# Optimization experiments

Measured on AMD Instinct MI355X. Metric: run time of the kernel, lower is better.

## Reference

```python
import jax, jax.numpy as jnp
import numpy as np

G, N, F, H, B, L = 4, 1024, 256, 256, 32, 4


def setup_inputs() -> dict:
    key = jax.random.key(0)
    ks = jax.random.split(key, 8)
    batch_xs = jax.random.normal(ks[0], (G, N, F), dtype=jnp.float32)
    # dense (preprocessed/normalized) adjacency; scale ~1/N keeps activations stable
    batch_as = jax.random.uniform(ks[1], (G, N, N), dtype=jnp.float32) / N
    w_in = jax.random.normal(ks[2], (F, H), dtype=jnp.float32) * 0.05
    b_in = jnp.zeros((H,), dtype=jnp.float32)
    gcn_w = jax.random.normal(ks[3], (L, H, H), dtype=jnp.float32) * 0.05
    gcn_b = jnp.zeros((L, H), dtype=jnp.float32)
    graph_idx = jax.random.randint(ks[4], (B,), 0, G)
    cp_mask = jax.random.randint(ks[5], (B, N), 0, 2).astype(bool)
    return {"batch_xs": batch_xs, "batch_as": batch_as, "w_in": w_in, "b_in": b_in,
            "gcn_w": gcn_w, "gcn_b": gcn_b, "graph_idx": graph_idx, "cp_mask": cp_mask}


def reference(batch_xs, batch_as, w_in, b_in, gcn_w, gcn_b, graph_idx, cp_mask):
    # gather_nd: select per-example graph features and adjacency
    X = batch_xs[graph_idx]          # [B, N, F]
    A = batch_as[graph_idx]          # [B, N, N]
    # GNN input dense layer (relu); dropout is identity at inference
    x = jax.nn.relu(X @ w_in + b_in)  # [B, N, H]
    res = x                           # residual from post-input activations
    # GCNConv stack: act(A @ x @ W + b); relu for all but final tanh layer
    for i in range(L - 1):
        x = jax.nn.relu(jnp.einsum('bnm,bmh->bnh', A, x) @ gcn_w[i] + gcn_b[i])
    x = jnp.tanh(jnp.einsum('bnm,bmh->bnh', A, x) @ gcn_w[L - 1] + gcn_b[L - 1])
    x = x + res
    # ragged boolean_mask + reduce_mean over nodes == masked mean
    m = cp_mask.astype(x.dtype)       # [B, N]
    denom = jnp.maximum(jnp.sum(m, axis=1, keepdims=True), 1.0)
    return jnp.sum(x * m[..., None], axis=1) / denom  # [B, H]
```

## Files before the change

kernel.cpp:

```cpp
#include <hip/hip_runtime.h>
#include <math.h>

#define G 4
#define NN 1024
#define FF 256
#define HH 256
#define BB 32
#define LL 4

typedef __attribute__((ext_vector_type(8))) short short8;
typedef __attribute__((ext_vector_type(8))) unsigned short ushort8;
typedef __attribute__((ext_vector_type(4))) unsigned short ushort4v;
typedef __attribute__((ext_vector_type(4))) float floatx4;

__device__ inline unsigned short f2bf(float f) {
  union { float f; unsigned u; } x; x.f = f;
  unsigned r = x.u + 0x7fffu + ((x.u >> 16) & 1u);
  return (unsigned short)(r >> 16);
}

template <int ACT, int AMODE, int OMODE, int SPLITK>
__global__ __launch_bounds__(256) void gemm(
    const void* __restrict__ Aptr, long aStride, long a2Off,
    const float* __restrict__ biasA,
    const unsigned short* __restrict__ Bt, long bStride,
    const float* __restrict__ biasC,
    unsigned short* __restrict__ outT,
    unsigned short* __restrict__ outBf,
    float* __restrict__ outF,
    int Kb, int ldA, int ldB) {
  __shared__ __align__(16) unsigned short As[64 * 72];
  __shared__ __align__(16) unsigned short Bs[64 * 72];

  const int z = blockIdx.z;
  const int g = (SPLITK == 2) ? (z & 3) : z;
  const int koff = (SPLITK == 2) ? (z >> 2) * Kb : 0;
  const int m0 = blockIdx.y * 64;
  const int n0 = blockIdx.x * 64;
  const int t = threadIdx.x;
  const int lane = t & 63, w = t >> 6;
  const int wm = w & 1, wn = w >> 1;
  const int l16 = lane & 15, quad = lane >> 4;

  const unsigned short* Bg = Bt + (long)g * bStride;

  ushort8 pa[2], pb[2];
  float4 pf[2][4];

  auto load_tile = [&](int tt) {
    const int kb = koff + tt * 64;
#pragma unroll
    for (int i = 0; i < 2; ++i) {
      const int q = t + i * 256;
      const int row = q >> 3, c8 = q & 7;
      if (AMODE == 0) {
        const unsigned short* Ab =
            (const unsigned short*)Aptr + (long)g * aStride;
        pa[i] = *(const ushort8*)&Ab[(long)(m0 + row) * ldA + kb + c8 * 8];
      } else {
        const float* Af = (const float*)Aptr + (long)g * aStride +
                          (long)(m0 + row) * ldA + kb + c8 * 8;
        pf[i][0] = *(const float4*)Af;
        pf[i][1] = *(const float4*)(Af + 4);
        if (AMODE == 2) {
          pf[i][2] = *(const float4*)(Af + a2Off);
          pf[i][3] = *(const float4*)(Af + a2Off + 4);
        }
      }
      pb[i] = *(const ushort8*)&Bg[(long)(n0 + row) * ldB + kb + c8 * 8];
    }
  };

  auto store_tile = [&](int tt) {
    const int kb = koff + tt * 64;
#pragma unroll
    for (int i = 0; i < 2; ++i) {
      const int q = t + i * 256;
      const int row = q >> 3, c8 = q & 7;
      ushort8 v;
      if (AMODE == 0) {
        v = pa[i];
      } else {
        float a[8] = {pf[i][0].x, pf[i][0].y, pf[i][0].z, pf[i][0].w,
                      pf[i][1].x, pf[i][1].y, pf[i][1].z, pf[i][1].w};
        if (AMODE == 2) {
          float a2[8] = {pf[i][2].x, pf[i][2].y, pf[i][2].z, pf[i][2].w,
                         pf[i][3].x, pf[i][3].y, pf[i][3].z, pf[i][3].w};
          float4 bb0 = *(const float4*)&biasA[kb + c8 * 8];
          float4 bb1 = *(const float4*)&biasA[kb + c8 * 8 + 4];
          float bb[8] = {bb0.x, bb0.y, bb0.z, bb0.w,
                         bb1.x, bb1.y, bb1.z, bb1.w};
#pragma unroll
          for (int j = 0; j < 8; ++j) a[j] = fmaxf(a[j] + a2[j] + bb[j], 0.f);
        }
#pragma unroll
        for (int j = 0; j < 8; ++j) v[j] = f2bf(a[j]);
      }
      *(ushort8*)&As[row * 72 + c8 * 8] = v;
      *(ushort8*)&Bs[row * 72 + c8 * 8] = pb[i];
    }
  };

  floatx4 acc[2][2];
#pragma unroll
  for (int i = 0; i < 2; ++i)
#pragma unroll
    for (int j = 0; j < 2; ++j) acc[i][j] = (floatx4){0.f, 0.f, 0.f, 0.f};

  const int nt = Kb / 64;
  load_tile(0);
  for (int tt = 0; tt < nt; ++tt) {
    __syncthreads();
    store_tile(tt);
    __syncthreads();
    if (tt + 1 < nt) load_tile(tt + 1);
#pragma unroll
    for (int kk = 0; kk < 64; kk += 32) {
      const int ko = kk + quad * 8;
      short8 a0 = *(const short8*)&As[(wm * 32 + l16) * 72 + ko];
      short8 a1 = *(const short8*)&As[(wm * 32 + 16 + l16) * 72 + ko];
      short8 b0 = *(const short8*)&Bs[(wn * 32 + l16) * 72 + ko];
      short8 b1 = *(const short8*)&Bs[(wn * 32 + 16 + l16) * 72 + ko];
      acc[0][0] = __builtin_amdgcn_mfma_f32_16x16x32_bf16(a0, b0, acc[0][0], 0, 0, 0);
      acc[0][1] = __builtin_amdgcn_mfma_f32_16x16x32_bf16(a0, b1, acc[0][1], 0, 0, 0);
      acc[1][0] = __builtin_amdgcn_mfma_f32_16x16x32_bf16(a1, b0, acc[1][0], 0, 0, 0);
      acc[1][1] = __builtin_amdgcn_mfma_f32_16x16x32_bf16(a1, b1, acc[1][1], 0, 0, 0);
    }
  }

  const int zc = (SPLITK == 2) ? z : g;
#pragma unroll
  for (int i = 0; i < 2; ++i) {
#pragma unroll
    for (int j = 0; j < 2; ++j) {
      const int n = n0 + wn * 32 + j * 16 + l16;
      const int mB = m0 + wm * 32 + i * 16 + quad * 4;
      const float bv = biasC ? biasC[n] : 0.f;
      ushort4v pv;
#pragma unroll
      for (int r = 0; r < 4; ++r) {
        float v = acc[i][j][r] + bv;
        if (ACT == 1) v = fmaxf(v, 0.f);
        if (OMODE & 4) outF[(long)zc * NN * HH + (long)(mB + r) * HH + n] = v;
        if (OMODE & 3) pv[r] = f2bf(v);
        if (OMODE & 2)
          outBf[(long)g * NN * HH + (long)(mB + r) * HH + n] = pv[r];
      }
      if (OMODE & 1)
        *(ushort4v*)&outT[(long)g * HH * NN + (long)n * NN + mB] = pv;
    }
  }
}

__global__ __launch_bounds__(256) void pre_kernel(
    const float* __restrict__ batch_as, unsigned short* __restrict__ Abf,
    const float* __restrict__ w_in, unsigned short* __restrict__ winT,
    const float* __restrict__ gcn_w, unsigned short* __restrict__ gwT,
    const void* __restrict__ mask_raw, float* __restrict__ fmask,
    float* __restrict__ denom, float* __restrict__ out) {
  const int b = blockIdx.x;
  const int t = threadIdx.x;
  if (b < 1024) {
    const long idx = ((long)b * 256 + t) * 16;
#pragma unroll
    for (int h = 0; h < 2; ++h) {
      float4 f0 = *(const float4*)&batch_as[idx + h * 8];
      float4 f1 = *(const float4*)&batch_as[idx + h * 8 + 4];
      ushort8 v;
      v[0] = f2bf(f0.x); v[1] = f2bf(f0.y); v[2] = f2bf(f0.z);
      v[3] = f2bf(f0.w); v[4] = f2bf(f1.x); v[5] = f2bf(f1.y);
      v[6] = f2bf(f1.z); v[7] = f2bf(f1.w);
      *(ushort8*)&Abf[idx + h * 8] = v;
    }
  } else if (b < 2304) {
    const int b2 = b - 1024;
    const int mat = b2 >> 8;
    const int rb = b2 & 255;
    const float* src = (mat == 0) ? w_in : gcn_w + (long)(mat - 1) * HH * HH;
    unsigned short* dst = (mat == 0) ? winT : gwT + (long)(mat - 1) * HH * HH;
    dst[rb * 256 + t] = f2bf(src[t * 256 + rb]);
  } else {
    const int bb = b - 2304;
    const unsigned char* bytes = (const unsigned char*)mask_raw;
    out[bb * HH + t] = 0.f;
    __shared__ int fmt;
    if (t == 0) {
      int any = 0;
      for (int i = 0; i < 256; ++i)
        if ((i & 3) && bytes[i]) any = 1;
      fmt = any ? 0 : 1;
    }
    __syncthreads();
    float cnt = 0.f;
    for (int n = t; n < NN; n += 256) {
      float v;
      if (fmt)
        v = ((const int*)mask_raw)[bb * NN + n] ? 1.f : 0.f;
      else
        v = bytes[bb * NN + n] ? 1.f : 0.f;
      fmask[bb * NN + n] = v;
      cnt += v;
    }
    __shared__ float red[256];
    red[t] = cnt;
    __syncthreads();
    for (int s = 128; s > 0; s >>= 1) {
      if (t < s) red[t] += red[t + s];
      __syncthreads();
    }
    if (t == 0) denom[bb] = fmaxf(red[0], 1.f);
  }
}

__global__ __launch_bounds__(256) void mean_kernel(
    const float* __restrict__ T0, const float* __restrict__ T1,
    const float* __restrict__ bias3, const float* __restrict__ h0f,
    const float* __restrict__ fmask, const float* __restrict__ denom,
    const int* __restrict__ gidx, float* __restrict__ out) {
  const int b = blockIdx.x >> 4;
  const int ch = blockIdx.x & 15;
  const int h = threadIdx.x;
  const int g = gidx[b];
  const long base = (long)g * NN * HH;
  const float bv = bias3[h];
  const int n0 = ch * 64;
  float s = 0.f;
  for (int n = n0; n < n0 + 64; ++n) {
    float m = fmask[b * NN + n];
    if (m != 0.f) {
      const long idx = base + (long)n * HH + h;
      s += tanhf(T0[idx] + T1[idx] + bv) + h0f[idx];
    }
  }
  atomicAdd(&out[b * HH + h], s / denom[b]);
}

extern "C" void kernel_launch(void* const* d_in, const int* in_sizes, int n_in,
                              void* d_out, int out_size, void* d_ws,
                              size_t ws_size, hipStream_t stream) {
  (void)in_sizes; (void)n_in; (void)out_size; (void)ws_size;
  const float* batch_xs = (const float*)d_in[0];
  const float* batch_as = (const float*)d_in[1];
  const float* w_in = (const float*)d_in[2];
  const float* b_in = (const float*)d_in[3];
  const float* gcn_w = (const float*)d_in[4];
  const float* gcn_b = (const float*)d_in[5];
  const int* graph_idx = (const int*)d_in[6];
  const void* cp_mask = d_in[7];
  float* out = (float*)d_out;

  char* p = (char*)d_ws;
  unsigned short* Abf = (unsigned short*)p;  p += (long)G * NN * NN * 2;
  unsigned short* winT = (unsigned short*)p; p += (long)FF * HH * 2;
  unsigned short* gwT = (unsigned short*)p;  p += (long)LL * HH * HH * 2;
  unsigned short* h0bf = (unsigned short*)p; p += (long)G * NN * HH * 2;
  unsigned short* yT = (unsigned short*)p;   p += (long)G * HH * NN * 2;
  float* h0f = (float*)p;                    p += (long)G * NN * HH * 4;
  float* Tsp = (float*)p;                    p += 8L * NN * HH * 4;
  float* fmask = (float*)p;                  p += (long)BB * NN * 4;
  float* denom = (float*)p;                  p += BB * 4;

  pre_kernel<<<2336, 256, 0, stream>>>(batch_as, Abf, w_in, winT, gcn_w, gwT,
                                       cp_mask, fmask, denom, out);

  {
    dim3 grid(HH / 64, NN / 64, G);
    gemm<1, 1, 6, 1><<<grid, 256, 0, stream>>>(
        batch_xs, (long)NN * FF, 0, nullptr, winT, 0, b_in,
        nullptr, h0bf, h0f, FF, FF, FF);
  }

  for (int l = 0; l < LL; ++l) {
    {
      dim3 grid(NN / 64, NN / 64 / 4, G);
      dim3 g1grid(HH / 64, NN / 64, G);
      if (l == 0)
        gemm<0, 0, 1, 1><<<g1grid, 256, 0, stream>>>(
            h0bf, (long)NN * HH, 0, nullptr, gwT + (long)l * HH * HH, 0,
            nullptr, yT, nullptr, nullptr, HH, HH, HH);
      else
        gemm<0, 2, 1, 1><<<g1grid, 256, 0, stream>>>(
            Tsp, (long)NN * HH, 4L * NN * HH, gcn_b + (long)(l - 1) * HH,
            gwT + (long)l * HH * HH, 0, nullptr, yT, nullptr, nullptr,
            HH, HH, HH);
    }
    {
      dim3 grid(HH / 64, NN / 64, 2 * G);
      gemm<0, 0, 4, 2><<<grid, 256, 0, stream>>>(
          Abf, (long)NN * NN, 0, nullptr, yT, (long)HH * NN, nullptr,
          nullptr, nullptr, Tsp, NN / 2, NN, NN);
    }
  }

  mean_kernel<<<BB * 16, 256, 0, stream>>>(
      Tsp, Tsp + 4L * NN * HH, gcn_b + 3L * HH, h0f, fmask, denom,
      graph_idx, out);
}
```

Measured before the change: 179.6 us.

## Fuse whole GCN pipeline into one cooperative persistent kernel with grid syncs

Replaces the sequence of separate launches (preconversion, input GEMM, per-layer GEMMs, mean) with a single cooperative kernel of 256 blocks that steps through the stages separated by grid.sync. The adjacency is no longer pre-converted to a bf16 copy; the A@Y GEMM reads fp32 adjacency and converts it while staging tiles. Split-K is dropped, so each block covers the full K=1024 and writes Tf directly. The intent is to remove launch overhead and the extra full pass over the adjacency, at the cost of fewer blocks per stage, grid-wide barriers, and a fallback multi-kernel path if the cooperative launch fails.

After: 509.7 us. 184% more time.

```diff
diff --git a/kernel.cpp b/kernel.cpp
--- a/kernel.cpp
+++ b/kernel.cpp
@@ -1,5 +1,8 @@
 #include <hip/hip_runtime.h>
+#include <hip/hip_cooperative_groups.h>
 #include <math.h>
+
+namespace cg = cooperative_groups;
 
 #define G 4
 #define NN 1024
@@ -19,82 +22,141 @@
   return (unsigned short)(r >> 16);
 }
 
-template <int ACT, int AMODE, int OMODE, int SPLITK>
-__global__ __launch_bounds__(256) void gemm(
-    const void* __restrict__ Aptr, long aStride, long a2Off,
-    const float* __restrict__ biasA,
-    const unsigned short* __restrict__ Bt, long bStride,
-    const float* __restrict__ biasC,
-    unsigned short* __restrict__ outT,
-    unsigned short* __restrict__ outBf,
-    float* __restrict__ outF,
-    int Kb, int ldA, int ldB) {
-  __shared__ __align__(16) unsigned short As[64 * 72];
-  __shared__ __align__(16) unsigned short Bs[64 * 72];
-
-  const int z = blockIdx.z;
-  const int g = (SPLITK == 2) ? (z & 3) : z;
-  const int koff = (SPLITK == 2) ? (z >> 2) * Kb : 0;
-  const int m0 = blockIdx.y * 64;
-  const int n0 = blockIdx.x * 64;
-  const int t = threadIdx.x;
+__device__ inline void mfma_tile(const unsigned short* As,
+                                 const unsigned short* Bs, floatx4 acc[2][2],
+                                 int l16, int quad, int wm, int wn) {
+#pragma unroll
+  for (int kk = 0; kk < 64; kk += 32) {
+    const int ko = kk + quad * 8;
+    short8 a0 = *(const short8*)&As[(wm * 32 + l16) * 72 + ko];
+    short8 a1 = *(const short8*)&As[(wm * 32 + 16 + l16) * 72 + ko];
+    short8 b0 = *(const short8*)&Bs[(wn * 32 + l16) * 72 + ko];
+    short8 b1 = *(const short8*)&Bs[(wn * 32 + 16 + l16) * 72 + ko];
+    acc[0][0] = __builtin_amdgcn_mfma_f32_16x16x32_bf16(a0, b0, acc[0][0], 0, 0, 0);
+    acc[0][1] = __builtin_amdgcn_mfma_f32_16x16x32_bf16(a0, b1, acc[0][1], 0, 0, 0);
+    acc[1][0] = __builtin_amdgcn_mfma_f32_16x16x32_bf16(a1, b0, acc[1][0], 0, 0, 0);
+    acc[1][1] = __builtin_amdgcn_mfma_f32_16x16x32_bf16(a1, b1, acc[1][1], 0, 0, 0);
+  }
+}
+
+__device__ void in_tile(int job, const float* __restrict__ X,
+                        const float* __restrict__ w_in,
+                        const float* __restrict__ b_in,
+                        unsigned short* __restrict__ h0bf,
+                        float* __restrict__ h0f, unsigned short* As,
+                        unsigned short* Bs, int t) {
+  const int nt_ = job & 3, mt = (job >> 2) & 15, g = job >> 6;
+  const int m0 = mt * 64, n0 = nt_ * 64;
   const int lane = t & 63, w = t >> 6;
   const int wm = w & 1, wn = w >> 1;
   const int l16 = lane & 15, quad = lane >> 4;
 
-  const unsigned short* Bg = Bt + (long)g * bStride;
-
-  ushort8 pa[2], pb[2];
-  float4 pf[2][4];
-
-  auto load_tile = [&](int tt) {
-    const int kb = koff + tt * 64;
+  floatx4 acc[2][2];
+#pragma unroll
+  for (int i = 0; i < 2; ++i)
+#pragma unroll
+    for (int j = 0; j < 2; ++j) acc[i][j] = (floatx4){0.f, 0.f, 0.f, 0.f};
+
+  for (int tt = 0; tt < 4; ++tt) {
+    const int kb = tt * 64;
+    __syncthreads();
 #pragma unroll
     for (int i = 0; i < 2; ++i) {
       const int q = t + i * 256;
       const int row = q >> 3, c8 = q & 7;
-      if (AMODE == 0) {
-        const unsigned short* Ab =
-            (const unsigned short*)Aptr + (long)g * aStride;
-        pa[i] = *(const ushort8*)&Ab[(long)(m0 + row) * ldA + kb + c8 * 8];
+      const float* Af = X + (long)g * NN * FF + (long)(m0 + row) * FF + kb + c8 * 8;
+      float4 f0 = *(const float4*)Af;
+      float4 f1 = *(const float4*)(Af + 4);
+      ushort8 v;
+      v[0] = f2bf(f0.x); v[1] = f2bf(f0.y); v[2] = f2bf(f0.z); v[3] = f2bf(f0.w);
+      v[4] = f2bf(f1.x); v[5] = f2bf(f1.y); v[6] = f2bf(f1.z); v[7] = f2bf(f1.w);
+      *(ushort8*)&As[row * 72 + c8 * 8] = v;
+    }
+    {
+      const int row = t >> 2;
+      const int c0 = (t & 3) * 16;
+#pragma unroll
+      for (int j = 0; j < 4; ++j) {
+        float4 f = *(const float4*)&w_in[(long)(kb + row) * HH + n0 + c0 + j * 4];
+        Bs[(c0 + j * 4 + 0) * 72 + row] = f2bf(f.x);
+        Bs[(c0 + j * 4 + 1) * 72 + row] = f2bf(f.y);
+        Bs[(c0 + j * 4 + 2) * 72 + row] = f2bf(f.z);
+        Bs[(c0 + j * 4 + 3) * 72 + row] = f2bf(f.w);
+      }
+    }
+    __syncthreads();
+    mfma_tile(As, Bs, acc, l16, quad, wm, wn);
+  }
+
+#pragma unroll
+  for (int i = 0; i < 2; ++i) {
+#pragma unroll
+    for (int j = 0; j < 2; ++j) {
+      const int n = n0 + wn * 32 + j * 16 + l16;
+      const int mB = m0 + wm * 32 + i * 16 + quad * 4;
+      const float bv = b_in[n];
+#pragma unroll
+      for (int r = 0; r < 4; ++r) {
+        const float v = fmaxf(acc[i][j][r] + bv, 0.f);
+        h0bf[(long)g * NN * HH + (long)(mB + r) * HH + n] = f2bf(v);
+        h0f[(long)g * NN * HH + (long)(mB + r) * HH + n] = v;
+      }
+    }
+  }
+}
+
+template <int AM>
+__device__ void g1_tile(int job, const unsigned short* __restrict__ Abf,
+                        const float* __restrict__ Tf,
+                        const float* __restrict__ biasA,
+                        const unsigned short* __restrict__ WT,
+                        unsigned short* __restrict__ yT, unsigned short* As,
+                        unsigned short* Bs, int t) {
+  const int nt_ = job & 3, mt = (job >> 2) & 15, g = job >> 6;
+  const int m0 = mt * 64, n0 = nt_ * 64;
+  const int lane = t & 63, w = t >> 6;
+  const int wm = w & 1, wn = w >> 1;
+  const int l16 = lane & 15, quad = lane >> 4;
+
+  const unsigned short* Ab = Abf + (long)g * NN * HH;
+  const float* A1 = Tf + (long)g * NN * HH;
+
+  ushort8 pa[2], pb[2];
+  float4 pf[2][2];
+
+  auto load_tile = [&](int tt) {
+    const int kb = tt * 64;
+#pragma unroll
+    for (int i = 0; i < 2; ++i) {
+      const int q = t + i * 256;
+      const int row = q >> 3, c8 = q & 7;
+      if (AM == 0) {
+        pa[i] = *(const ushort8*)&Ab[(long)(m0 + row) * HH + kb + c8 * 8];
       } else {
-        const float* Af = (const float*)Aptr + (long)g * aStride +
-                          (long)(m0 + row) * ldA + kb + c8 * 8;
-        pf[i][0] = *(const float4*)Af;
-        pf[i][1] = *(const float4*)(Af + 4);
-        if (AMODE == 2) {
-          pf[i][2] = *(const float4*)(Af + a2Off);
-          pf[i][3] = *(const float4*)(Af + a2Off + 4);
-        }
+        const float* a1 = A1 + (long)(m0 + row) * HH + kb + c8 * 8;
+        pf[i][0] = *(const float4*)a1;
+        pf[i][1] = *(const float4*)(a1 + 4);
       }
-      pb[i] = *(const ushort8*)&Bg[(long)(n0 + row) * ldB + kb + c8 * 8];
+      pb[i] = *(const ushort8*)&WT[(long)(n0 + row) * HH + kb + c8 * 8];
     }
   };
-
   auto store_tile = [&](int tt) {
-    const int kb = koff + tt * 64;
+    const int kb = tt * 64;
 #pragma unroll
     for (int i = 0; i < 2; ++i) {
       const int q = t + i * 256;
       const int row = q >> 3, c8 = q & 7;
       ushort8 v;
-      if (AMODE == 0) {
+      if (AM == 0) {
         v = pa[i];
       } else {
         float a[8] = {pf[i][0].x, pf[i][0].y, pf[i][0].z, pf[i][0].w,
                       pf[i][1].x, pf[i][1].y, pf[i][1].z, pf[i][1].w};
-        if (AMODE == 2) {
-          float a2[8] = {pf[i][2].x, pf[i][2].y, pf[i][2].z, pf[i][2].w,
-                         pf[i][3].x, pf[i][3].y, pf[i][3].z, pf[i][3].w};
-          float4 bb0 = *(const float4*)&biasA[kb + c8 * 8];
-          float4 bb1 = *(const float4*)&biasA[kb + c8 * 8 + 4];
-          float bb[8] = {bb0.x, bb0.y, bb0.z, bb0.w,
-                         bb1.x, bb1.y, bb1.z, bb1.w};
-#pragma unroll
-          for (int j = 0; j < 8; ++j) a[j] = fmaxf(a[j] + a2[j] + bb[j], 0.f);
-        }
-#pragma unroll
-        for (int j = 0; j < 8; ++j) v[j] = f2bf(a[j]);
+        float4 bb0 = *(const float4*)&biasA[kb + c8 * 8];
+        float4 bb1 = *(const float4*)&biasA[kb + c8 * 8 + 4];
+        float bb[8] = {bb0.x, bb0.y, bb0.z, bb0.w, bb1.x, bb1.y, bb1.z, bb1.w};
+#pragma unroll
+        for (int j = 0; j < 8; ++j) v[j] = f2bf(fmaxf(a[j] + bb[j], 0.f));
       }
       *(ushort8*)&As[row * 72 + c8 * 8] = v;
       *(ushort8*)&Bs[row * 72 + c8 * 8] = pb[i];
@@ -107,132 +169,266 @@
 #pragma unroll
     for (int j = 0; j < 2; ++j) acc[i][j] = (floatx4){0.f, 0.f, 0.f, 0.f};
 
-  const int nt = Kb / 64;
   load_tile(0);
-  for (int tt = 0; tt < nt; ++tt) {
+  for (int tt = 0; tt < 4; ++tt) {
     __syncthreads();
     store_tile(tt);
     __syncthreads();
-    if (tt + 1 < nt) load_tile(tt + 1);
-#pragma unroll
-    for (int kk = 0; kk < 64; kk += 32) {
-      const int ko = kk + quad * 8;
-      short8 a0 = *(const short8*)&As[(wm * 32 + l16) * 72 + ko];
-      short8 a1 = *(const short8*)&As[(wm * 32 + 16 + l16) * 72 + ko];
-      short8 b0 = *(const short8*)&Bs[(wn * 32 + l16) * 72 + ko];
-      short8 b1 = *(const short8*)&Bs[(wn * 32 + 16 + l16) * 72 + ko];
-      acc[0][0] = __builtin_amdgcn_mfma_f32_16x16x32_bf16(a0, b0, acc[0][0], 0, 0, 0);
-      acc[0][1] = __builtin_amdgcn_mfma_f32_16x16x32_bf16(a0, b1, acc[0][1], 0, 0, 0);
-      acc[1][0] = __builtin_amdgcn_mfma_f32_16x16x32_bf16(a1, b0, acc[1][0], 0, 0, 0);
-      acc[1][1] = __builtin_amdgcn_mfma_f32_16x16x32_bf16(a1, b1, acc[1][1], 0, 0, 0);
-    }
-  }
-
-  const int zc = (SPLITK == 2) ? z : g;
+    if (tt + 1 < 4) load_tile(tt + 1);
+    mfma_tile(As, Bs, acc, l16, quad, wm, wn);
+  }
+
 #pragma unroll
   for (int i = 0; i < 2; ++i) {
 #pragma unroll
     for (int j = 0; j < 2; ++j) {
       const int n = n0 + wn * 32 + j * 16 + l16;
       const int mB = m0 + wm * 32 + i * 16 + quad * 4;
-      const float bv = biasC ? biasC[n] : 0.f;
       ushort4v pv;
 #pragma unroll
-      for (int r = 0; r < 4; ++r) {
-        float v = acc[i][j][r] + bv;
-        if (ACT == 1) v = fmaxf(v, 0.f);
-        if (OMODE & 4) outF[(long)zc * NN * HH + (long)(mB + r) * HH + n] = v;
-        if (OMODE & 3) pv[r] = f2bf(v);
-        if (OMODE & 2)
-          outBf[(long)g * NN * HH + (long)(mB + r) * HH + n] = pv[r];
-      }
-      if (OMODE & 1)
-        *(ushort4v*)&outT[(long)g * HH * NN + (long)n * NN + mB] = pv;
-    }
-  }
-}
-
-__global__ __launch_bounds__(256) void pre_kernel(
-    const float* __restrict__ batch_as, unsigned short* __restrict__ Abf,
-    const float* __restrict__ w_in, unsigned short* __restrict__ winT,
-    const float* __restrict__ gcn_w, unsigned short* __restrict__ gwT,
-    const void* __restrict__ mask_raw, float* __restrict__ fmask,
-    float* __restrict__ denom, float* __restrict__ out) {
-  const int b = blockIdx.x;
-  const int t = threadIdx.x;
-  if (b < 1024) {
-    const long idx = ((long)b * 256 + t) * 16;
-#pragma unroll
-    for (int h = 0; h < 2; ++h) {
-      float4 f0 = *(const float4*)&batch_as[idx + h * 8];
-      float4 f1 = *(const float4*)&batch_as[idx + h * 8 + 4];
+      for (int r = 0; r < 4; ++r) pv[r] = f2bf(acc[i][j][r]);
+      *(ushort4v*)&yT[(long)g * HH * NN + (long)n * NN + mB] = pv;
+    }
+  }
+}
+
+__device__ void g2_tile(int job, const float* __restrict__ Aall,
+                        const unsigned short* __restrict__ yT,
+                        float* __restrict__ Tf, unsigned short* As,
+                        unsigned short* Bs, int t) {
+  const int nt_ = job & 3, mt = (job >> 2) & 15, g = job >> 6;
+  const int m0 = mt * 64, n0 = nt_ * 64;
+  const int lane = t & 63, w = t >> 6;
+  const int wm = w & 1, wn = w >> 1;
+  const int l16 = lane & 15, quad = lane >> 4;
+
+  const float* Ag = Aall + (long)g * NN * NN;
+  const unsigned short* Bg = yT + (long)g * HH * NN;
+
+  float4 pf[2][2];
+  ushort8 pb[2];
+
+  auto load_tile = [&](int tt) {
+    const int kb = tt * 64;
+#pragma unroll
+    for (int i = 0; i < 2; ++i) {
+      const int q = t + i * 256;
+      const int row = q >> 3, c8 = q & 7;
+      const float* a = Ag + (long)(m0 + row) * NN + kb + c8 * 8;
+      pf[i][0] = *(const float4*)a;
+      pf[i][1] = *(const float4*)(a + 4);
+      pb[i] = *(const ushort8*)&Bg[(long)(n0 + row) * NN + kb + c8 * 8];
+    }
+  };
+  auto store_tile = [&]() {
+#pragma unroll
+    for (int i = 0; i < 2; ++i) {
+      const int q = t + i * 256;
+      const int row = q >> 3, c8 = q & 7;
       ushort8 v;
-      v[0] = f2bf(f0.x); v[1] = f2bf(f0.y); v[2] = f2bf(f0.z);
-      v[3] = f2bf(f0.w); v[4] = f2bf(f1.x); v[5] = f2bf(f1.y);
-      v[6] = f2bf(f1.z); v[7] = f2bf(f1.w);
-      *(ushort8*)&Abf[idx + h * 8] = v;
-    }
-  } else if (b < 2304) {
-    const int b2 = b - 1024;
-    const int mat = b2 >> 8;
-    const int rb = b2 & 255;
-    const float* src = (mat == 0) ? w_in : gcn_w + (long)(mat - 1) * HH * HH;
-    unsigned short* dst = (mat == 0) ? winT : gwT + (long)(mat - 1) * HH * HH;
-    dst[rb * 256 + t] = f2bf(src[t * 256 + rb]);
-  } else {
-    const int bb = b - 2304;
-    const unsigned char* bytes = (const unsigned char*)mask_raw;
-    out[bb * HH + t] = 0.f;
-    __shared__ int fmt;
-    if (t == 0) {
-      int any = 0;
-      for (int i = 0; i < 256; ++i)
-        if ((i & 3) && bytes[i]) any = 1;
-      fmt = any ? 0 : 1;
-    }
-    __syncthreads();
-    float cnt = 0.f;
-    for (int n = t; n < NN; n += 256) {
-      float v;
-      if (fmt)
-        v = ((const int*)mask_raw)[bb * NN + n] ? 1.f : 0.f;
-      else
-        v = bytes[bb * NN + n] ? 1.f : 0.f;
-      fmask[bb * NN + n] = v;
-      cnt += v;
-    }
-    __shared__ float red[256];
-    red[t] = cnt;
-    __syncthreads();
-    for (int s = 128; s > 0; s >>= 1) {
-      if (t < s) red[t] += red[t + s];
-      __syncthreads();
-    }
-    if (t == 0) denom[bb] = fmaxf(red[0], 1.f);
-  }
-}
-
-__global__ __launch_bounds__(256) void mean_kernel(
-    const float* __restrict__ T0, const float* __restrict__ T1,
-    const float* __restrict__ bias3, const float* __restrict__ h0f,
-    const float* __restrict__ fmask, const float* __restrict__ denom,
-    const int* __restrict__ gidx, float* __restrict__ out) {
-  const int b = blockIdx.x >> 4;
-  const int ch = blockIdx.x & 15;
-  const int h = threadIdx.x;
+      v[0] = f2bf(pf[i][0].x); v[1] = f2bf(pf[i][0].y);
+      v[2] = f2bf(pf[i][0].z); v[3] = f2bf(pf[i][0].w);
+      v[4] = f2bf(pf[i][1].x); v[5] = f2bf(pf[i][1].y);
+      v[6] = f2bf(pf[i][1].z); v[7] = f2bf(pf[i][1].w);
+      *(ushort8*)&As[row * 72 + c8 * 8] = v;
+      *(ushort8*)&Bs[row * 72 + c8 * 8] = pb[i];
+    }
+  };
+
+  floatx4 acc[2][2];
+#pragma unroll
+  for (int i = 0; i < 2; ++i)
+#pragma unroll
+    for (int j = 0; j < 2; ++j) acc[i][j] = (floatx4){0.f, 0.f, 0.f, 0.f};
+
+  load_tile(0);
+  for (int tt = 0; tt < 16; ++tt) {
+    __syncthreads();
+    store_tile();
+    __syncthreads();
+    if (tt + 1 < 16) load_tile(tt + 1);
+    mfma_tile(As, Bs, acc, l16, quad, wm, wn);
+  }
+
+#pragma unroll
+  for (int i = 0; i < 2; ++i) {
+#pragma unroll
+    for (int j = 0; j < 2; ++j) {
+      const int n = n0 + wn * 32 + j * 16 + l16;
+      const int mB = m0 + wm * 32 + i * 16 + quad * 4;
+#pragma unroll
+      for (int r = 0; r < 4; ++r)
+        Tf[(long)g * NN * HH + (long)(mB + r) * HH + n] = acc[i][j][r];
+    }
+  }
+}
+
+__device__ void mask_job(int b, const void* __restrict__ cp_mask,
+                         float* __restrict__ fmask, float* __restrict__ denom,
+                         int t) {
+  const unsigned char* bytes = (const unsigned char*)cp_mask;
+  __shared__ int fmt;
+  __shared__ float red[256];
+  if (t == 0) {
+    int any = 0;
+    for (int i = 0; i < 256; ++i)
+      if ((i & 3) && bytes[i]) any = 1;
+    fmt = any ? 0 : 1;
+  }
+  __syncthreads();
+  float cnt = 0.f;
+  for (int n = t; n < NN; n += 256) {
+    float v;
+    if (fmt)
+      v = ((const int*)cp_mask)[b * NN + n] ? 1.f : 0.f;
+    else
+      v = bytes[b * NN + n] ? 1.f : 0.f;
+    fmask[b * NN + n] = v;
+    cnt += v;
+  }
+  red[t] = cnt;
+  __syncthreads();
+  for (int s = 128; s > 0; s >>= 1) {
+    if (t < s) red[t] += red[t + s];
+    __syncthreads();
+  }
+  if (t == 0) denom[b] = fmaxf(red[0], 1.f);
+}
+
+__device__ void gw_job(int j, const float* __restrict__ gcn_w,
+                       unsigned short* __restrict__ gwT, int t) {
+  const int l = j >> 4, r0 = (j & 15) * 16;
+  const float* src = gcn_w + (long)l * HH * HH;
+  unsigned short* dst = gwT + (long)l * HH * HH;
+  unsigned short vv[16];
+#pragma unroll
+  for (int rr = 0; rr < 16; ++rr) vv[rr] = f2bf(src[(long)(r0 + rr) * HH + t]);
+  *(ushort8*)&dst[(long)t * HH + r0] = *(ushort8*)&vv[0];
+  *(ushort8*)&dst[(long)t * HH + r0 + 8] = *(ushort8*)&vv[8];
+}
+
+__device__ void mean_job(int job, const float* __restrict__ Tf,
+                         const float* __restrict__ bias3,
+                         const float* __restrict__ h0f,
+                         const float* __restrict__ fmask,
+                         const float* __restrict__ denom,
+                         const int* __restrict__ gidx,
+                         float* __restrict__ out, int t) {
+  const int b = job >> 3, ch = job & 7;
+  const int h = t;
   const int g = gidx[b];
   const long base = (long)g * NN * HH;
   const float bv = bias3[h];
-  const int n0 = ch * 64;
+  const float* T = Tf + base;
+  const float* r0 = h0f + base;
+  const int n0 = ch * 128;
   float s = 0.f;
-  for (int n = n0; n < n0 + 64; ++n) {
+  for (int n = n0; n < n0 + 128; ++n) {
     float m = fmask[b * NN + n];
     if (m != 0.f) {
-      const long idx = base + (long)n * HH + h;
-      s += tanhf(T0[idx] + T1[idx] + bv) + h0f[idx];
+      const long idx = (long)n * HH + h;
+      s += tanhf(T[idx] + bv) + r0[idx];
     }
   }
   atomicAdd(&out[b * HH + h], s / denom[b]);
+}
+
+__global__ __launch_bounds__(256) void mega(
+    const float* __restrict__ batch_xs, const float* __restrict__ batch_as,
+    const float* __restrict__ w_in, const float* __restrict__ b_in,
+    const float* __restrict__ gcn_w, const float* __restrict__ gcn_b,
+    const int* __restrict__ graph_idx, const void* __restrict__ cp_mask,
+    float* __restrict__ out, char* __restrict__ ws) {
+  __shared__ __align__(16) unsigned short As[64 * 72];
+  __shared__ __align__(16) unsigned short Bs[64 * 72];
+
+  char* p = ws;
+  unsigned short* gwT = (unsigned short*)p;  p += (long)LL * HH * HH * 2;
+  unsigned short* h0bf = (unsigned short*)p; p += (long)G * NN * HH * 2;
+  unsigned short* yT = (unsigned short*)p;   p += (long)G * HH * NN * 2;
+  float* h0f = (float*)p;                    p += (long)G * NN * HH * 4;
+  float* Tf = (float*)p;                     p += (long)G * NN * HH * 4;
+  float* fmask = (float*)p;                  p += (long)BB * NN * 4;
+  float* denom = (float*)p;                  p += BB * 4;
+
+  const int t = threadIdx.x;
+  const int bid = blockIdx.x;
+  cg::grid_group grid = cg::this_grid();
+
+  for (int job = bid; job < 353; job += 256) {
+    if (job < 256) {
+      in_tile(job, batch_xs, w_in, b_in, h0bf, h0f, As, Bs, t);
+    } else if (job < 288) {
+      mask_job(job - 256, cp_mask, fmask, denom, t);
+    } else if (job == 288) {
+      for (int i = 0; i < 32; ++i) out[i * 256 + t] = 0.f;
+    } else {
+      gw_job(job - 289, gcn_w, gwT, t);
+    }
+  }
+  grid.sync();
+
+  for (int l = 0; l < LL; ++l) {
+    if (l == 0)
+      g1_tile<0>(bid, h0bf, nullptr, nullptr, gwT, yT, As, Bs, t);
+    else
+      g1_tile<2>(bid, nullptr, Tf, gcn_b + (long)(l - 1) * HH,
+                 gwT + (long)l * HH * HH, yT, As, Bs, t);
+    grid.sync();
+    g2_tile(bid, batch_as, yT, Tf, As, Bs, t);
+    grid.sync();
+  }
+
+  mean_job(bid, Tf, gcn_b + 3L * HH, h0f, fmask, denom, graph_idx, out, t);
+}
+
+__global__ __launch_bounds__(256) void fb_misc(
+    const float* __restrict__ gcn_w, unsigned short* __restrict__ gwT,
+    const void* __restrict__ cp_mask, float* __restrict__ fmask,
+    float* __restrict__ denom, float* __restrict__ out) {
+  const int b = blockIdx.x, t = threadIdx.x;
+  if (b < 32) {
+    mask_job(b, cp_mask, fmask, denom, t);
+  } else if (b == 32) {
+    for (int i = 0; i < 32; ++i) out[i * 256 + t] = 0.f;
+  } else {
+    gw_job(b - 33, gcn_w, gwT, t);
+  }
+}
+
+__global__ __launch_bounds__(256) void fb_in(
+    const float* __restrict__ X, const float* __restrict__ w_in,
+    const float* __restrict__ b_in, unsigned short* __restrict__ h0bf,
+    float* __restrict__ h0f) {
+  __shared__ __align__(16) unsigned short As[64 * 72];
+  __shared__ __align__(16) unsigned short Bs[64 * 72];
+  in_tile(blockIdx.x, X, w_in, b_in, h0bf, h0f, As, Bs, threadIdx.x);
+}
+
+template <int AM>
+__global__ __launch_bounds__(256) void fb_g1(
+    const unsigned short* __restrict__ Abf, const float* __restrict__ Tf,
+    const float* __restrict__ biasA, const unsigned short* __restrict__ WT,
+    unsigned short* __restrict__ yT) {
+  __shared__ __align__(16) unsigned short As[64 * 72];
+  __shared__ __align__(16) unsigned short Bs[64 * 72];
+  g1_tile<AM>(blockIdx.x, Abf, Tf, biasA, WT, yT, As, Bs, threadIdx.x);
+}
+
+__global__ __launch_bounds__(256) void fb_g2(
+    const float* __restrict__ Aall, const unsigned short* __restrict__ yT,
+    float* __restrict__ Tf) {
+  __shared__ __align__(16) unsigned short As[64 * 72];
+  __shared__ __align__(16) unsigned short Bs[64 * 72];
+  g2_tile(blockIdx.x, Aall, yT, Tf, As, Bs, threadIdx.x);
+}
+
+__global__ __launch_bounds__(256) void fb_mean(
+    const float* __restrict__ Tf, const float* __restrict__ bias3,
+    const float* __restrict__ h0f, const float* __restrict__ fmask,
+    const float* __restrict__ denom, const int* __restrict__ gidx,
+    float* __restrict__ out) {
+  mean_job(blockIdx.x, Tf, bias3, h0f, fmask, denom, gidx, out, threadIdx.x);
 }
 
 extern "C" void kernel_launch(void* const* d_in, const int* in_sizes, int n_in,
@@ -248,51 +444,34 @@
   const int* graph_idx = (const int*)d_in[6];
   const void* cp_mask = d_in[7];
   float* out = (float*)d_out;
-
-  char* p = (char*)d_ws;
-  unsigned short* Abf = (unsigned short*)p;  p += (long)G * NN * NN * 2;
-  unsigned short* winT = (unsigned short*)p; p += (long)FF * HH * 2;
-  unsigned short* gwT = (unsigned short*)p;  p += (long)LL * HH * HH * 2;
-  unsigned short* h0bf = (unsigned short*)p; p += (long)G * NN * HH * 2;
-  unsigned short* yT = (unsigned short*)p;   p += (long)G * HH * NN * 2;
-  float* h0f = (float*)p;                    p += (long)G * NN * HH * 4;
-  float* Tsp = (float*)p;                    p += 8L * NN * HH * 4;
-  float* fmask = (float*)p;                  p += (long)BB * NN * 4;
-  float* denom = (float*)p;                  p += BB * 4;
-
-  pre_kernel<<<2336, 256, 0, stream>>>(batch_as, Abf, w_in, winT, gcn_w, gwT,
-                                       cp_mask, fmask, denom, out);
-
-  {
-    dim3 grid(HH / 64, NN / 64, G);
-    gemm<1, 1, 6, 1><<<grid, 256, 0, stream>>>(
-        batch_xs, (long)NN * FF, 0, nullptr, winT, 0, b_in,
-        nullptr, h0bf, h0f, FF, FF, FF);
-  }
-
-  for (int l = 0; l < LL; ++l) {
-    {
-      dim3 grid(NN / 64, NN / 64 / 4, G);
-      dim3 g1grid(HH / 64, NN / 64, G);
+  char* ws = (char*)d_ws;
+
+  void* args[] = {&batch_xs, &batch_as, &w_in, &b_in, &gcn_w, &gcn_b,
+                  &graph_idx, &cp_mask, &out, &ws};
+  hipError_t err = hipLaunchCooperativeKernel((void*)mega, dim3(256),
+                                              dim3(256), args, 0, stream);
+  if (err != hipSuccess) {
+    char* p = ws;
+    unsigned short* gwT = (unsigned short*)p;  p += (long)LL * HH * HH * 2;
+    unsigned short* h0bf = (unsigned short*)p; p += (long)G * NN * HH * 2;
+    unsigned short* yT = (unsigned short*)p;   p += (long)G * HH * NN * 2;
+    float* h0f = (float*)p;                    p += (long)G * NN * HH * 4;
+    float* Tf = (float*)p;                     p += (long)G * NN * HH * 4;
+    float* fmask = (float*)p;                  p += (long)BB * NN * 4;
+    float* denom = (float*)p;                  p += BB * 4;
+
+    fb_misc<<<97, 256, 0, stream>>>(gcn_w, gwT, cp_mask, fmask, denom, out);
+    fb_in<<<256, 256, 0, stream>>>(batch_xs, w_in, b_in, h0bf, h0f);
+    for (int l = 0; l < LL; ++l) {
       if (l == 0)
-        gemm<0, 0, 1, 1><<<g1grid, 256, 0, stream>>>(
-            h0bf, (long)NN * HH, 0, nullptr, gwT + (long)l * HH * HH, 0,
-            nullptr, yT, nullptr, nullptr, HH, HH, HH);
+        fb_g1<0><<<256, 256, 0, stream>>>(h0bf, nullptr, nullptr, gwT, yT);
       else
-        gemm<0, 2, 1, 1><<<g1grid, 256, 0, stream>>>(
-            Tsp, (long)NN * HH, 4L * NN * HH, gcn_b + (long)(l - 1) * HH,
-            gwT + (long)l * HH * HH, 0, nullptr, yT, nullptr, nullptr,
-            HH, HH, HH);
-    }
-    {
-      dim3 grid(HH / 64, NN / 64, 2 * G);
-      gemm<0, 0, 4, 2><<<grid, 256, 0, stream>>>(
-          Abf, (long)NN * NN, 0, nullptr, yT, (long)HH * NN, nullptr,
-          nullptr, nullptr, Tsp, NN / 2, NN, NN);
-    }
-  }
-
-  mean_kernel<<<BB * 16, 256, 0, stream>>>(
-      Tsp, Tsp + 4L * NN * HH, gcn_b + 3L * HH, h0f, fmask, denom,
-      graph_idx, out);
-}
+        fb_g1<2><<<256, 256, 0, stream>>>(nullptr, Tf,
+                                          gcn_b + (long)(l - 1) * HH,
+                                          gwT + (long)l * HH * HH, yT);
+      fb_g2<<<256, 256, 0, stream>>>(batch_as, yT, Tf);
+    }
+    fb_mean<<<256, 256, 0, stream>>>(Tf, gcn_b + 3L * HH, h0f, fmask, denom,
+                                     graph_idx, out);
+  }
+}
```
